# Kernel tuning notes

Hardware: AMD Instinct MI355X
Metric: run time of the kernel (lower is better)

The kernel has to match this reference:

```python
import jax, jax.numpy as jnp
import numpy as np

# Qwen3-VL-MoE text experts (training path): token permute -> grouped GEMM
# (gate_up) -> SwiGLU -> grouped GEMM (down) -> token unpermute + prob combine.
# Routing is generated perfectly balanced (each expert receives exactly M/E
# expanded tokens) so the grouped GEMM over the sorted token buffer is exactly
# a batched matmul over E contiguous groups -- same math as npu_grouped_matmul.

E, H, D, T, K = 32, 2048, 768, 4096, 8  # experts, hidden, moe_intermediate, tokens, top_k
M = T * K                                # expanded rows


def setup_inputs() -> dict:
    key = jax.random.key(0)
    k1, k2, k3, k4, k5 = jax.random.split(key, 5)
    hidden_states = jax.random.normal(k1, (T, H), dtype=jnp.float32)
    routing_weights = jax.nn.softmax(jax.random.normal(k2, (T, E), dtype=jnp.float32), axis=-1)
    # balanced expert assignment: each expert id appears exactly M // E times
    flat = jnp.tile(jnp.arange(E, dtype=jnp.int32), M // E)
    router_indices = jax.random.permutation(k3, flat).reshape(T, K)
    gate_up_proj = jax.random.normal(k4, (E, H, 2 * D), dtype=jnp.float32) * 0.02
    down_proj = jax.random.normal(k5, (E, D, H), dtype=jnp.float32) * 0.02
    return {
        "hidden_states": hidden_states,
        "routing_weights": routing_weights,
        "router_indices": router_indices,
        "gate_up_proj": gate_up_proj,
        "down_proj": down_proj,
    }


def reference(hidden_states, routing_weights, router_indices, gate_up_proj, down_proj):
    n_tok, hid = hidden_states.shape
    n_exp = gate_up_proj.shape[0]
    top_k = router_indices.shape[1]
    n_rows = n_tok * top_k
    grp = n_rows // n_exp  # balanced group size

    # --- npu_moe_token_permute: sort expanded (token, slot) rows by expert id
    flat_experts = router_indices.reshape(-1)            # (M,)
    order = jnp.argsort(flat_experts)                    # stable sort by expert
    permuted = hidden_states[order // top_k]             # (M, H)

    # --- grouped GEMM #1 (gate_up): balanced groups -> batched matmul
    xg = permuted.reshape(n_exp, grp, hid)               # (E, g, H)
    gate_up = jnp.einsum('egh,ehd->egd', xg, gate_up_proj)  # (E, g, 2D)

    # --- npu_swiglu(dim=-1): silu(first half) * second half
    gate, up = jnp.split(gate_up, 2, axis=-1)
    act = jax.nn.silu(gate) * up                         # (E, g, D)

    # --- grouped GEMM #2 (down)
    out = jnp.einsum('egd,edh->egh', act, down_proj).reshape(n_rows, hid)

    # --- npu_moe_token_unpermute: invert permutation, combine with probs
    inv = jnp.argsort(order)
    expanded = out[inv].reshape(n_tok, top_k, hid)       # (T, K, H)
    probs = jnp.take_along_axis(routing_weights, router_indices, axis=1)  # (T, K)
    return jnp.einsum('tkh,tk->th', expanded, probs)     # (T, H)
```

## Files before the change

### kernel.cpp

```cpp
#include <hip/hip_runtime.h>
#include <hip/hip_bf16.h>
#include <cstdint>


#define E_   32
#define H_   2048
#define D_   768
#define T_   4096
#define K_   8
#define M_   (T_ * K_)
#define G_   (M_ / E_)
#define GU2  (2 * D_)

typedef unsigned short u16;
typedef short bf16x8 __attribute__((ext_vector_type(8)));
typedef float f32x4 __attribute__((ext_vector_type(4)));
typedef unsigned short u16x2 __attribute__((ext_vector_type(2)));
typedef unsigned short u16x8 __attribute__((ext_vector_type(8)));

__device__ __forceinline__ u16 f2bf(float f) {
  unsigned u = __float_as_uint(f);
  u += 0x7FFFu + ((u >> 16) & 1u);
  return (u16)(u >> 16);
}
__device__ __forceinline__ float bf2f(u16 v) {
  return __uint_as_float(((unsigned)v) << 16);
}

#define GLOAD16(g, l) __builtin_amdgcn_global_load_lds(                        \
    (const __attribute__((address_space(1))) void*)(g),                        \
    (__attribute__((address_space(3))) void*)(l), 16, 0, 0)

#define VM8()   asm volatile("s_waitcnt vmcnt(8)" ::: "memory")
#define VM4()   asm volatile("s_waitcnt vmcnt(4)" ::: "memory")
#define VM0()   asm volatile("s_waitcnt vmcnt(0)" ::: "memory")
#define LGKM0() asm volatile("s_waitcnt lgkmcnt(0)" ::: "memory")
#define SCHB()  __builtin_amdgcn_sched_barrier(0)
#define BAR()   __builtin_amdgcn_s_barrier()

__global__ __launch_bounds__(256) void cvt_hidden(const float* __restrict__ in,
                                                  u16* __restrict__ out) {
  const int i = blockIdx.x * 256 + threadIdx.x;
  const float4 v = ((const float4*)in)[i];
  u16x2 a; a.x = f2bf(v.x); a.y = f2bf(v.y);
  u16x2 b; b.x = f2bf(v.z); b.y = f2bf(v.w);
  *(u16x2*)&out[(size_t)i * 4]     = a;
  *(u16x2*)&out[(size_t)i * 4 + 2] = b;
}

__global__ __launch_bounds__(256) void transpose_cvt(const float* __restrict__ in,
                                                     u16* __restrict__ out,
                                                     int R, int C, int mode) {
  __shared__ u16 tl[64 * 72];
  const int b = blockIdx.z;
  const int c0 = blockIdx.x * 64, r0 = blockIdx.y * 64;
  const int tid = threadIdx.x;
  const float* ip = in + ((size_t)b * R + r0) * C + c0;
  const int rr4 = tid >> 4;
  const int cc4 = (tid & 15) * 4;
#pragma unroll
  for (int p = 0; p < 4; ++p) {
    const int r = p * 16 + rr4;
    const float4 v = *(const float4*)&ip[(size_t)r * C + cc4];
    tl[(cc4 + 0) * 72 + r] = f2bf(v.x);
    tl[(cc4 + 1) * 72 + r] = f2bf(v.y);
    tl[(cc4 + 2) * 72 + r] = f2bf(v.z);
    tl[(cc4 + 3) * 72 + r] = f2bf(v.w);
  }
  __syncthreads();
  const int rs = (tid & 7) * 8;
#pragma unroll
  for (int q = 0; q < 2; ++q) {
    const int c = q * 32 + (tid >> 3);
    const int gc = c0 + c;
    int rr;
    if (mode == 1) {
      const int j = (gc < D_) ? gc : (gc - D_);
      rr = (j >> 4) * 32 + ((gc < D_) ? 0 : 16) + (j & 15);
    } else {
      rr = gc;
    }
    const u16x8 v = *(const u16x8*)&tl[c * 72 + rs];
    *(u16x8*)&out[((size_t)b * C + rr) * R + r0 + rs] = v;
  }
}

__global__ __launch_bounds__(256) void build_perm_fast(const int* __restrict__ ridx,
                                                       int* __restrict__ perm,
                                                       int* __restrict__ gcnt) {
  __shared__ int lc[E_];
  __shared__ int lb[E_];
  const int tid = threadIdx.x;
  if (tid < E_) lc[tid] = 0;
  __syncthreads();
  const int i = blockIdx.x * 256 + tid;
  const int e = ridx[i];
  const int p = atomicAdd(&lc[e], 1);
  __syncthreads();
  if (tid < E_) lb[tid] = atomicAdd(&gcnt[tid], lc[tid]);
  __syncthreads();
  perm[e * G_ + lb[e] + p] = i;
}

__global__ __launch_bounds__(512, 2) void gemm1_swiglu(
    const u16* __restrict__ hid, const u16* __restrict__ gup,
    const int* __restrict__ perm, u16* __restrict__ act) {
  __shared__ u16 As[4][8192];
  __shared__ u16 Bs[4][8192];
  const int NT = H_ / 32;

  const int nwg = 6 * 4 * E_;
  const int wid = (blockIdx.x % 8) * (nwg / 8) + blockIdx.x / 8;
  const int e = wid / 24;
  const int mb = (wid / 6) % 4;
  const int nb = wid % 6;

  const int tid = threadIdx.x;
  const int lane = tid & 63, w = tid >> 6;
  const int wr = w >> 2, wc = w & 3;

  const int srow = tid >> 2, schunk = tid & 3;
  const u16* pA[2]; const u16* pB[2];
#pragma unroll
  for (int q = 0; q < 2; ++q) {
    const int r = q * 128 + srow;
    const int cg = (schunk ^ ((r >> 1) & 3)) * 8;
    const int token = perm[e * G_ + mb * 256 + r] >> 3;
    pA[q] = hid + (size_t)token * H_ + cg;
    pB[q] = gup + ((size_t)e * GU2 + nb * 256 + r) * H_ + cg;
  }

  int aoff[8], boff[4];
  {
    const int l15 = lane & 15, hk = lane >> 4;
#pragma unroll
    for (int m = 0; m < 8; ++m) {
      const int rA = wr * 128 + m * 16 + l15;
      aoff[m] = rA * 32 + ((hk ^ ((rA >> 1) & 3)) * 8);
    }
#pragma unroll
    for (int n = 0; n < 4; ++n) {
      const int rB = wc * 64 + n * 16 + l15;
      boff[n] = rB * 32 + ((hk ^ ((rB >> 1) & 3)) * 8);
    }
  }

  f32x4 acc[8][4];
#pragma unroll
  for (int m = 0; m < 8; ++m)
#pragma unroll
    for (int n = 0; n < 4; ++n) acc[m][n] = (f32x4){0.f, 0.f, 0.f, 0.f};

  GLOAD16(pA[0], &As[0][tid * 8]);      GLOAD16(pA[1], &As[0][4096 + tid * 8]);
  GLOAD16(pB[0], &Bs[0][tid * 8]);      GLOAD16(pB[1], &Bs[0][4096 + tid * 8]);
  GLOAD16(pA[0] + 32, &As[1][tid * 8]); GLOAD16(pA[1] + 32, &As[1][4096 + tid * 8]);
  GLOAD16(pB[0] + 32, &Bs[1][tid * 8]); GLOAD16(pB[1] + 32, &Bs[1][4096 + tid * 8]);
  GLOAD16(pA[0] + 64, &As[2][tid * 8]); GLOAD16(pA[1] + 64, &As[2][4096 + tid * 8]);
  GLOAD16(pB[0] + 64, &Bs[2][tid * 8]); GLOAD16(pB[1] + 64, &Bs[2][4096 + tid * 8]);
  VM8(); BAR(); SCHB();

#pragma unroll 4
  for (int t = 0; t < NT; ++t) {
    const int slot = t & 3, ts = (t + 3) & 3;
    const bool st = (t + 3) < NT;
    const u16* Ab = As[slot]; const u16* Bb = Bs[slot];
    bf16x8 av[4], bv[4];
#pragma unroll
    for (int n = 0; n < 4; ++n) bv[n] = *(const bf16x8*)&Bb[boff[n]];
#pragma unroll
    for (int m = 0; m < 4; ++m) av[m] = *(const bf16x8*)&Ab[aoff[m]];
    if (st) {
      GLOAD16(pA[0] + (t + 3) * 32, &As[ts][tid * 8]);
      GLOAD16(pA[1] + (t + 3) * 32, &As[ts][4096 + tid * 8]);
    }
    SCHB(); LGKM0(); SCHB();
    __builtin_amdgcn_s_setprio(1);
#pragma unroll
    for (int m = 0; m < 4; ++m)
#pragma unroll
      for (int n = 0; n < 4; ++n)
        acc[m][n] = __builtin_amdgcn_mfma_f32_16x16x32_bf16(av[m], bv[n],
                                                            acc[m][n], 0, 0, 0);
    __builtin_amdgcn_s_setprio(0);
    SCHB();
#pragma unroll
    for (int m = 0; m < 4; ++m) av[m] = *(const bf16x8*)&Ab[aoff[m + 4]];
    if (st) {
      GLOAD16(pB[0] + (t + 3) * 32, &Bs[ts][tid * 8]);
      GLOAD16(pB[1] + (t + 3) * 32, &Bs[ts][4096 + tid * 8]);
    }
    SCHB(); LGKM0(); SCHB();
    __builtin_amdgcn_s_setprio(1);
#pragma unroll
    for (int m = 0; m < 4; ++m)
#pragma unroll
      for (int n = 0; n < 4; ++n)
        acc[m + 4][n] = __builtin_amdgcn_mfma_f32_16x16x32_bf16(av[m], bv[n],
                                                                acc[m + 4][n], 0, 0, 0);
    __builtin_amdgcn_s_setprio(0);
    SCHB();
    if (t + 3 < NT)      { VM8(); }
    else if (t + 2 < NT) { VM4(); }
    else                 { VM0(); }
    BAR(); SCHB();
  }

  const int lrow = (lane >> 4) * 4, lcol = lane & 15;
#pragma unroll
  for (int m = 0; m < 8; ++m)
#pragma unroll
    for (int p = 0; p < 2; ++p)
#pragma unroll
      for (int r = 0; r < 4; ++r) {
        const float g = acc[m][2 * p][r];
        const float u = acc[m][2 * p + 1][r];
        const float a_ = g / (1.f + __expf(-g)) * u;
        const int row = mb * 256 + wr * 128 + m * 16 + lrow + r;
        const int dcol = (nb * 8 + wc * 2 + p) * 16 + lcol;
        act[((size_t)e * G_ + row) * D_ + dcol] = f2bf(a_);
      }
}

__global__ __launch_bounds__(512, 2) void gemm2_scatter(
    const u16* __restrict__ act, const u16* __restrict__ dwn,
    const int* __restrict__ perm, u16* __restrict__ expo) {
  __shared__ u16 As[4][8192];
  __shared__ u16 Bs[4][8192];
  const int NT = D_ / 32;

  const int nwg = 8 * 4 * E_;
  const int wid = (blockIdx.x % 8) * (nwg / 8) + blockIdx.x / 8;
  const int e = wid / 32;
  const int mb = (wid / 8) % 4;
  const int nb = wid % 8;

  const int tid = threadIdx.x;
  const int lane = tid & 63, w = tid >> 6;
  const int wr = w >> 2, wc = w & 3;

  const int srow = tid >> 2, schunk = tid & 3;
  const u16* pA[2]; const u16* pB[2];
#pragma unroll
  for (int q = 0; q < 2; ++q) {
    const int r = q * 128 + srow;
    const int cg = (schunk ^ ((r >> 1) & 3)) * 8;
    pA[q] = act + ((size_t)e * G_ + mb * 256 + r) * D_ + cg;
    pB[q] = dwn + ((size_t)e * H_ + nb * 256 + r) * D_ + cg;
  }

  int aoff[8], boff[4];
  {
    const int l15 = lane & 15, hk = lane >> 4;
#pragma unroll
    for (int m = 0; m < 8; ++m) {
      const int rA = wr * 128 + m * 16 + l15;
      aoff[m] = rA * 32 + ((hk ^ ((rA >> 1) & 3)) * 8);
    }
#pragma unroll
    for (int n = 0; n < 4; ++n) {
      const int rB = wc * 64 + n * 16 + l15;
      boff[n] = rB * 32 + ((hk ^ ((rB >> 1) & 3)) * 8);
    }
  }

  f32x4 acc[8][4];
#pragma unroll
  for (int m = 0; m < 8; ++m)
#pragma unroll
    for (int n = 0; n < 4; ++n) acc[m][n] = (f32x4){0.f, 0.f, 0.f, 0.f};

  GLOAD16(pA[0], &As[0][tid * 8]);      GLOAD16(pA[1], &As[0][4096 + tid * 8]);
  GLOAD16(pB[0], &Bs[0][tid * 8]);      GLOAD16(pB[1], &Bs[0][4096 + tid * 8]);
  GLOAD16(pA[0] + 32, &As[1][tid * 8]); GLOAD16(pA[1] + 32, &As[1][4096 + tid * 8]);
  GLOAD16(pB[0] + 32, &Bs[1][tid * 8]); GLOAD16(pB[1] + 32, &Bs[1][4096 + tid * 8]);
  GLOAD16(pA[0] + 64, &As[2][tid * 8]); GLOAD16(pA[1] + 64, &As[2][4096 + tid * 8]);
  GLOAD16(pB[0] + 64, &Bs[2][tid * 8]); GLOAD16(pB[1] + 64, &Bs[2][4096 + tid * 8]);
  VM8(); BAR(); SCHB();

#pragma unroll 4
  for (int t = 0; t < NT; ++t) {
    const int slot = t & 3, ts = (t + 3) & 3;
    const bool st = (t + 3) < NT;
    const u16* Ab = As[slot]; const u16* Bb = Bs[slot];
    bf16x8 av[4], bv[4];
#pragma unroll
    for (int n = 0; n < 4; ++n) bv[n] = *(const bf16x8*)&Bb[boff[n]];
#pragma unroll
    for (int m = 0; m < 4; ++m) av[m] = *(const bf16x8*)&Ab[aoff[m]];
    if (st) {
      GLOAD16(pA[0] + (t + 3) * 32, &As[ts][tid * 8]);
      GLOAD16(pA[1] + (t + 3) * 32, &As[ts][4096 + tid * 8]);
    }
    SCHB(); LGKM0(); SCHB();
    __builtin_amdgcn_s_setprio(1);
#pragma unroll
    for (int m = 0; m < 4; ++m)
#pragma unroll
      for (int n = 0; n < 4; ++n)
        acc[m][n] = __builtin_amdgcn_mfma_f32_16x16x32_bf16(av[m], bv[n],
                                                            acc[m][n], 0, 0, 0);
    __builtin_amdgcn_s_setprio(0);
    SCHB();
#pragma unroll
    for (int m = 0; m < 4; ++m) av[m] = *(const bf16x8*)&Ab[aoff[m + 4]];
    if (st) {
      GLOAD16(pB[0] + (t + 3) * 32, &Bs[ts][tid * 8]);
      GLOAD16(pB[1] + (t + 3) * 32, &Bs[ts][4096 + tid * 8]);
    }
    SCHB(); LGKM0(); SCHB();
    __builtin_amdgcn_s_setprio(1);
#pragma unroll
    for (int m = 0; m < 4; ++m)
#pragma unroll
      for (int n = 0; n < 4; ++n)
        acc[m + 4][n] = __builtin_amdgcn_mfma_f32_16x16x32_bf16(av[m], bv[n],
                                                                acc[m + 4][n], 0, 0, 0);
    __builtin_amdgcn_s_setprio(0);
    SCHB();
    if (t + 3 < NT)      { VM8(); }
    else if (t + 2 < NT) { VM4(); }
    else                 { VM0(); }
    BAR(); SCHB();
  }

  const int lrow = (lane >> 4) * 4, lcol = lane & 15;
#pragma unroll
  for (int m = 0; m < 8; ++m)
#pragma unroll
    for (int r = 0; r < 4; ++r) {
      const int dst = e * G_ + mb * 256 + wr * 128 + m * 16 + lrow + r;
      const int src = perm[dst];
      u16* orow = expo + (size_t)src * H_ + nb * 256 + wc * 64;
#pragma unroll
      for (int n = 0; n < 4; ++n)
        orow[n * 16 + lcol] = f2bf(acc[m][n][r]);
    }
}

__global__ __launch_bounds__(256) void combine(const u16* __restrict__ expo,
                                               const int* __restrict__ ridx,
                                               const float* __restrict__ rw,
                                               float* __restrict__ out) {
  __shared__ float pr[K_];
  const int t = blockIdx.x;
  if (threadIdx.x < K_)
    pr[threadIdx.x] = rw[t * E_ + ridx[t * K_ + threadIdx.x]];
  __syncthreads();
  const int h0 = threadIdx.x * 8;
  float r[8] = {0.f, 0.f, 0.f, 0.f, 0.f, 0.f, 0.f, 0.f};
#pragma unroll
  for (int k = 0; k < K_; ++k) {
    const float p = pr[k];
    const u16x8 v = *(const u16x8*)&expo[((size_t)(t * K_ + k)) * H_ + h0];
#pragma unroll
    for (int j = 0; j < 8; ++j) r[j] += p * bf2f(v[j]);
  }
  float4 o0 = {r[0], r[1], r[2], r[3]};
  float4 o1 = {r[4], r[5], r[6], r[7]};
  *(float4*)&out[(size_t)t * H_ + h0]     = o0;
  *(float4*)&out[(size_t)t * H_ + h0 + 4] = o1;
}

extern "C" void kernel_launch(void* const* d_in, const int* in_sizes, int n_in,
                              void* d_out, int out_size, void* d_ws, size_t ws_size,
                              hipStream_t stream) {
  const float* hidden = (const float*)d_in[0];
  const float* rw     = (const float*)d_in[1];
  const int*   ridx   = (const int*)d_in[2];
  const float* gup_f  = (const float*)d_in[3];
  const float* dwn_f  = (const float*)d_in[4];
  float* out = (float*)d_out;

  char* ws = (char*)d_ws;
  size_t off = 0;
  auto alloc = [&](size_t bytes) -> void* {
    void* p = ws + off;
    off += (bytes + 255) & ~(size_t)255;
    return p;
  };
  u16*   hid_bf = (u16*)alloc((size_t)T_ * H_ * 2);
  u16*   gup_t  = (u16*)alloc((size_t)E_ * GU2 * H_ * 2);
  u16*   dwn_t  = (u16*)alloc((size_t)E_ * H_ * D_ * 2);
  u16*   act    = (u16*)alloc((size_t)M_ * D_ * 2);
  u16*   expo   = (u16*)alloc((size_t)M_ * H_ * 2);
  int*   perm   = (int*)alloc((size_t)M_ * 4);
  int*   gcnt   = (int*)alloc((size_t)E_ * 4);
  if (off > ws_size) return;

  hipMemsetAsync(gcnt, 0, E_ * sizeof(int), stream);
  cvt_hidden<<<(T_ * H_ / 4) / 256, 256, 0, stream>>>(hidden, hid_bf);
  transpose_cvt<<<dim3(GU2 / 64, H_ / 64, E_), 256, 0, stream>>>(gup_f, gup_t, H_, GU2, 1);
  transpose_cvt<<<dim3(H_ / 64, D_ / 64, E_), 256, 0, stream>>>(dwn_f, dwn_t, D_, H_, 0);
  build_perm_fast<<<M_ / 256, 256, 0, stream>>>(ridx, perm, gcnt);
  gemm1_swiglu<<<6 * 4 * E_, 512, 0, stream>>>(hid_bf, gup_t, perm, act);
  gemm2_scatter<<<8 * 4 * E_, 512, 0, stream>>>(act, dwn_t, perm, expo);
  combine<<<T_, 256, 0, stream>>>(expo, ridx, rw, out);
}
```

Before: 528.7 us.

## Software-pipeline LDS fragment reads with register double-buffering in both GEMMs

Restructures the main loop of both grouped GEMM kernels so the A/B fragments for the next K-tile are read from LDS into a second register set while the current tile's MFMAs run, ping-ponging between two register buffers. All four global-to-LDS prefetches for tile t+3 are now issued together at the start of each iteration, and the vmcnt waits are adjusted to match. The aim is to hide LDS read latency behind matrix math. The cost is more live VGPRs for the doubled fragment registers, which may lower occupancy or cause spills. The loop also assumes an even tile count.

```diff
diff --git a/kernel.cpp b/kernel.cpp
--- a/kernel.cpp
+++ b/kernel.cpp
@@ -31,12 +31,46 @@
     (const __attribute__((address_space(1))) void*)(g),                        \
     (__attribute__((address_space(3))) void*)(l), 16, 0, 0)
 
-#define VM8()   asm volatile("s_waitcnt vmcnt(8)" ::: "memory")
 #define VM4()   asm volatile("s_waitcnt vmcnt(4)" ::: "memory")
 #define VM0()   asm volatile("s_waitcnt vmcnt(0)" ::: "memory")
 #define LGKM0() asm volatile("s_waitcnt lgkmcnt(0)" ::: "memory")
 #define SCHB()  __builtin_amdgcn_sched_barrier(0)
 #define BAR()   __builtin_amdgcn_s_barrier()
+
+#define TILE_BODY(tc, AVC, BVC, AVN, BVN)                                      \
+  {                                                                            \
+    LGKM0(); SCHB();                                                           \
+    if ((tc) + 3 < NT) {                                                       \
+      const int s_ = ((tc) + 3) & 3;                                           \
+      GLOAD16(pA[0] + ((tc) + 3) * 32, &As[s_][tid * 8]);                      \
+      GLOAD16(pA[1] + ((tc) + 3) * 32, &As[s_][4096 + tid * 8]);               \
+      GLOAD16(pB[0] + ((tc) + 3) * 32, &Bs[s_][tid * 8]);                      \
+      GLOAD16(pB[1] + ((tc) + 3) * 32, &Bs[s_][4096 + tid * 8]);               \
+    }                                                                          \
+    __builtin_amdgcn_s_setprio(1);                                             \
+    _Pragma("unroll") for (int m_ = 0; m_ < 4; ++m_)                           \
+      _Pragma("unroll") for (int n_ = 0; n_ < 4; ++n_)                         \
+        acc[m_][n_] = __builtin_amdgcn_mfma_f32_16x16x32_bf16(                 \
+            AVC[m_], BVC[n_], acc[m_][n_], 0, 0, 0);                           \
+    __builtin_amdgcn_s_setprio(0);                                             \
+    if ((tc) + 1 < NT) {                                                       \
+      const u16* Abn_ = As[((tc) + 1) & 3];                                    \
+      const u16* Bbn_ = Bs[((tc) + 1) & 3];                                    \
+      _Pragma("unroll") for (int n_ = 0; n_ < 4; ++n_)                         \
+        BVN[n_] = *(const bf16x8*)&Bbn_[boff[n_]];                             \
+      _Pragma("unroll") for (int m_ = 0; m_ < 8; ++m_)                         \
+        AVN[m_] = *(const bf16x8*)&Abn_[aoff[m_]];                             \
+    }                                                                          \
+    __builtin_amdgcn_s_setprio(1);                                             \
+    _Pragma("unroll") for (int m_ = 0; m_ < 4; ++m_)                           \
+      _Pragma("unroll") for (int n_ = 0; n_ < 4; ++n_)                         \
+        acc[m_ + 4][n_] = __builtin_amdgcn_mfma_f32_16x16x32_bf16(             \
+            AVC[m_ + 4], BVC[n_], acc[m_ + 4][n_], 0, 0, 0);                   \
+    __builtin_amdgcn_s_setprio(0);                                             \
+    SCHB();                                                                    \
+    if ((tc) + 3 < NT) { VM4(); } else { VM0(); }                              \
+    BAR(); SCHB();                                                             \
+  }
 
 __global__ __launch_bounds__(256) void cvt_hidden(const float* __restrict__ in,
                                                   u16* __restrict__ out) {
@@ -157,52 +191,21 @@
   GLOAD16(pB[0] + 32, &Bs[1][tid * 8]); GLOAD16(pB[1] + 32, &Bs[1][4096 + tid * 8]);
   GLOAD16(pA[0] + 64, &As[2][tid * 8]); GLOAD16(pA[1] + 64, &As[2][4096 + tid * 8]);
   GLOAD16(pB[0] + 64, &Bs[2][tid * 8]); GLOAD16(pB[1] + 64, &Bs[2][4096 + tid * 8]);
-  VM8(); BAR(); SCHB();
-
-#pragma unroll 4
-  for (int t = 0; t < NT; ++t) {
-    const int slot = t & 3, ts = (t + 3) & 3;
-    const bool st = (t + 3) < NT;
-    const u16* Ab = As[slot]; const u16* Bb = Bs[slot];
-    bf16x8 av[4], bv[4];
-#pragma unroll
-    for (int n = 0; n < 4; ++n) bv[n] = *(const bf16x8*)&Bb[boff[n]];
-#pragma unroll
-    for (int m = 0; m < 4; ++m) av[m] = *(const bf16x8*)&Ab[aoff[m]];
-    if (st) {
-      GLOAD16(pA[0] + (t + 3) * 32, &As[ts][tid * 8]);
-      GLOAD16(pA[1] + (t + 3) * 32, &As[ts][4096 + tid * 8]);
-    }
-    SCHB(); LGKM0(); SCHB();
-    __builtin_amdgcn_s_setprio(1);
-#pragma unroll
-    for (int m = 0; m < 4; ++m)
-#pragma unroll
-      for (int n = 0; n < 4; ++n)
-        acc[m][n] = __builtin_amdgcn_mfma_f32_16x16x32_bf16(av[m], bv[n],
-                                                            acc[m][n], 0, 0, 0);
-    __builtin_amdgcn_s_setprio(0);
-    SCHB();
-#pragma unroll
-    for (int m = 0; m < 4; ++m) av[m] = *(const bf16x8*)&Ab[aoff[m + 4]];
-    if (st) {
-      GLOAD16(pB[0] + (t + 3) * 32, &Bs[ts][tid * 8]);
-      GLOAD16(pB[1] + (t + 3) * 32, &Bs[ts][4096 + tid * 8]);
-    }
-    SCHB(); LGKM0(); SCHB();
-    __builtin_amdgcn_s_setprio(1);
-#pragma unroll
-    for (int m = 0; m < 4; ++m)
-#pragma unroll
-      for (int n = 0; n < 4; ++n)
-        acc[m + 4][n] = __builtin_amdgcn_mfma_f32_16x16x32_bf16(av[m], bv[n],
-                                                                acc[m + 4][n], 0, 0, 0);
-    __builtin_amdgcn_s_setprio(0);
-    SCHB();
-    if (t + 3 < NT)      { VM8(); }
-    else if (t + 2 < NT) { VM4(); }
-    else                 { VM0(); }
-    BAR(); SCHB();
+  VM4(); BAR(); SCHB();
+
+  bf16x8 av0[8], bv0[4], av1[8], bv1[4];
+  {
+    const u16* Ab = As[0]; const u16* Bb = Bs[0];
+#pragma unroll
+    for (int n = 0; n < 4; ++n) bv0[n] = *(const bf16x8*)&Bb[boff[n]];
+#pragma unroll
+    for (int m = 0; m < 8; ++m) av0[m] = *(const bf16x8*)&Ab[aoff[m]];
+  }
+
+#pragma unroll 2
+  for (int t = 0; t < NT; t += 2) {
+    TILE_BODY(t,     av0, bv0, av1, bv1);
+    TILE_BODY(t + 1, av1, bv1, av0, bv0);
   }
 
   const int lrow = (lane >> 4) * 4, lcol = lane & 15;
@@ -275,52 +278,21 @@
   GLOAD16(pB[0] + 32, &Bs[1][tid * 8]); GLOAD16(pB[1] + 32, &Bs[1][4096 + tid * 8]);
   GLOAD16(pA[0] + 64, &As[2][tid * 8]); GLOAD16(pA[1] + 64, &As[2][4096 + tid * 8]);
   GLOAD16(pB[0] + 64, &Bs[2][tid * 8]); GLOAD16(pB[1] + 64, &Bs[2][4096 + tid * 8]);
-  VM8(); BAR(); SCHB();
-
-#pragma unroll 4
-  for (int t = 0; t < NT; ++t) {
-    const int slot = t & 3, ts = (t + 3) & 3;
-    const bool st = (t + 3) < NT;
-    const u16* Ab = As[slot]; const u16* Bb = Bs[slot];
-    bf16x8 av[4], bv[4];
-#pragma unroll
-    for (int n = 0; n < 4; ++n) bv[n] = *(const bf16x8*)&Bb[boff[n]];
-#pragma unroll
-    for (int m = 0; m < 4; ++m) av[m] = *(const bf16x8*)&Ab[aoff[m]];
-    if (st) {
-      GLOAD16(pA[0] + (t + 3) * 32, &As[ts][tid * 8]);
-      GLOAD16(pA[1] + (t + 3) * 32, &As[ts][4096 + tid * 8]);
-    }
-    SCHB(); LGKM0(); SCHB();
-    __builtin_amdgcn_s_setprio(1);
-#pragma unroll
-    for (int m = 0; m < 4; ++m)
-#pragma unroll
-      for (int n = 0; n < 4; ++n)
-        acc[m][n] = __builtin_amdgcn_mfma_f32_16x16x32_bf16(av[m], bv[n],
-                                                            acc[m][n], 0, 0, 0);
-    __builtin_amdgcn_s_setprio(0);
-    SCHB();
-#pragma unroll
-    for (int m = 0; m < 4; ++m) av[m] = *(const bf16x8*)&Ab[aoff[m + 4]];
-    if (st) {
-      GLOAD16(pB[0] + (t + 3) * 32, &Bs[ts][tid * 8]);
-      GLOAD16(pB[1] + (t + 3) * 32, &Bs[ts][4096 + tid * 8]);
-    }
-    SCHB(); LGKM0(); SCHB();
-    __builtin_amdgcn_s_setprio(1);
-#pragma unroll
-    for (int m = 0; m < 4; ++m)
-#pragma unroll
-      for (int n = 0; n < 4; ++n)
-        acc[m + 4][n] = __builtin_amdgcn_mfma_f32_16x16x32_bf16(av[m], bv[n],
-                                                                acc[m + 4][n], 0, 0, 0);
-    __builtin_amdgcn_s_setprio(0);
-    SCHB();
-    if (t + 3 < NT)      { VM8(); }
-    else if (t + 2 < NT) { VM4(); }
-    else                 { VM0(); }
-    BAR(); SCHB();
+  VM4(); BAR(); SCHB();
+
+  bf16x8 av0[8], bv0[4], av1[8], bv1[4];
+  {
+    const u16* Ab = As[0]; const u16* Bb = Bs[0];
+#pragma unroll
+    for (int n = 0; n < 4; ++n) bv0[n] = *(const bf16x8*)&Bb[boff[n]];
+#pragma unroll
+    for (int m = 0; m < 8; ++m) av0[m] = *(const bf16x8*)&Ab[aoff[m]];
+  }
+
+#pragma unroll 2
+  for (int t = 0; t < NT; t += 2) {
+    TILE_BODY(t,     av0, bv0, av1, bv1);
+    TILE_BODY(t + 1, av1, bv1, av0, bv0);
   }
 
   const int lrow = (lane >> 4) * 4, lcol = lane & 15;
```

Result: slower. 1.794 ms (+239.3%).

## Fuse prep kernels and overlap down_proj transpose with gate_up GEMM

Applied to the files above, without the earlier changes.

The hidden-state cast, the gate_up transpose/convert and the permutation build are merged into one launch that picks its role from the block index. The down_proj transpose/convert moves into gemm1 as four extra producer warps, so its memory traffic runs alongside the MFMA loop. To stay in lockstep, the producer warps issue the same number of block barriers as the compute warps. This saves several launches and hides the transpose's bandwidth cost, but raises the block size to 768 threads and adds LDS, which may constrain registers or contend for memory bandwidth with the GEMM.

```diff
diff --git a/kernel.cpp b/kernel.cpp
--- a/kernel.cpp
+++ b/kernel.cpp
@@ -38,187 +38,221 @@
 #define SCHB()  __builtin_amdgcn_sched_barrier(0)
 #define BAR()   __builtin_amdgcn_s_barrier()
 
-__global__ __launch_bounds__(256) void cvt_hidden(const float* __restrict__ in,
-                                                  u16* __restrict__ out) {
-  const int i = blockIdx.x * 256 + threadIdx.x;
-  const float4 v = ((const float4*)in)[i];
-  u16x2 a; a.x = f2bf(v.x); a.y = f2bf(v.y);
-  u16x2 b; b.x = f2bf(v.z); b.y = f2bf(v.w);
-  *(u16x2*)&out[(size_t)i * 4]     = a;
-  *(u16x2*)&out[(size_t)i * 4 + 2] = b;
-}
-
-__global__ __launch_bounds__(256) void transpose_cvt(const float* __restrict__ in,
-                                                     u16* __restrict__ out,
-                                                     int R, int C, int mode) {
+__global__ __launch_bounds__(256) void prep_fused(
+    const float* __restrict__ hidden, u16* __restrict__ hid_bf,
+    const float* __restrict__ gup_f, u16* __restrict__ gup_t,
+    const int* __restrict__ ridx, int* __restrict__ perm,
+    int* __restrict__ gcnt) {
   __shared__ u16 tl[64 * 72];
-  const int b = blockIdx.z;
-  const int c0 = blockIdx.x * 64, r0 = blockIdx.y * 64;
-  const int tid = threadIdx.x;
-  const float* ip = in + ((size_t)b * R + r0) * C + c0;
-  const int rr4 = tid >> 4;
-  const int cc4 = (tid & 15) * 4;
-#pragma unroll
-  for (int p = 0; p < 4; ++p) {
-    const int r = p * 16 + rr4;
-    const float4 v = *(const float4*)&ip[(size_t)r * C + cc4];
-    tl[(cc4 + 0) * 72 + r] = f2bf(v.x);
-    tl[(cc4 + 1) * 72 + r] = f2bf(v.y);
-    tl[(cc4 + 2) * 72 + r] = f2bf(v.z);
-    tl[(cc4 + 3) * 72 + r] = f2bf(v.w);
-  }
-  __syncthreads();
-  const int rs = (tid & 7) * 8;
-#pragma unroll
-  for (int q = 0; q < 2; ++q) {
-    const int c = q * 32 + (tid >> 3);
-    const int gc = c0 + c;
-    int rr;
-    if (mode == 1) {
-      const int j = (gc < D_) ? gc : (gc - D_);
-      rr = (j >> 4) * 32 + ((gc < D_) ? 0 : 16) + (j & 15);
-    } else {
-      rr = gc;
-    }
-    const u16x8 v = *(const u16x8*)&tl[c * 72 + rs];
-    *(u16x8*)&out[((size_t)b * C + rr) * R + r0 + rs] = v;
-  }
-}
-
-__global__ __launch_bounds__(256) void build_perm_fast(const int* __restrict__ ridx,
-                                                       int* __restrict__ perm,
-                                                       int* __restrict__ gcnt) {
   __shared__ int lc[E_];
   __shared__ int lb[E_];
+  const int bid = blockIdx.x;
   const int tid = threadIdx.x;
-  if (tid < E_) lc[tid] = 0;
-  __syncthreads();
-  const int i = blockIdx.x * 256 + tid;
-  const int e = ridx[i];
-  const int p = atomicAdd(&lc[e], 1);
-  __syncthreads();
-  if (tid < E_) lb[tid] = atomicAdd(&gcnt[tid], lc[tid]);
-  __syncthreads();
-  perm[e * G_ + lb[e] + p] = i;
-}
-
-__global__ __launch_bounds__(512, 2) void gemm1_swiglu(
+  if (bid < 24576) {
+    const int bx = bid % 24, by = (bid / 24) % 32, bz = bid / 768;
+    const int c0 = bx * 64, r0 = by * 64;
+    const float* ip = gup_f + ((size_t)bz * H_ + r0) * GU2 + c0;
+    const int rr4 = tid >> 4;
+    const int cc4 = (tid & 15) * 4;
+#pragma unroll
+    for (int p = 0; p < 4; ++p) {
+      const int r = p * 16 + rr4;
+      const float4 v = *(const float4*)&ip[(size_t)r * GU2 + cc4];
+      tl[(cc4 + 0) * 72 + r] = f2bf(v.x);
+      tl[(cc4 + 1) * 72 + r] = f2bf(v.y);
+      tl[(cc4 + 2) * 72 + r] = f2bf(v.z);
+      tl[(cc4 + 3) * 72 + r] = f2bf(v.w);
+    }
+    __syncthreads();
+    const int rs = (tid & 7) * 8;
+#pragma unroll
+    for (int q = 0; q < 2; ++q) {
+      const int c = q * 32 + (tid >> 3);
+      const int gc = c0 + c;
+      const int j = (gc < D_) ? gc : (gc - D_);
+      const int rr = (j >> 4) * 32 + ((gc < D_) ? 0 : 16) + (j & 15);
+      const u16x8 v = *(const u16x8*)&tl[c * 72 + rs];
+      *(u16x8*)&gup_t[((size_t)bz * GU2 + rr) * H_ + r0 + rs] = v;
+    }
+  } else if (bid < 24576 + 8192) {
+    const int i = (bid - 24576) * 256 + tid;
+    const float4 v = ((const float4*)hidden)[i];
+    u16x2 a; a.x = f2bf(v.x); a.y = f2bf(v.y);
+    u16x2 b; b.x = f2bf(v.z); b.y = f2bf(v.w);
+    *(u16x2*)&hid_bf[(size_t)i * 4]     = a;
+    *(u16x2*)&hid_bf[(size_t)i * 4 + 2] = b;
+  } else {
+    const int blk = bid - 32768;
+    if (tid < E_) lc[tid] = 0;
+    __syncthreads();
+    const int i = blk * 256 + tid;
+    const int e = ridx[i];
+    const int p = atomicAdd(&lc[e], 1);
+    __syncthreads();
+    if (tid < E_) lb[tid] = atomicAdd(&gcnt[tid], lc[tid]);
+    __syncthreads();
+    perm[e * G_ + lb[e] + p] = i;
+  }
+}
+
+__global__ __launch_bounds__(768, 1) void gemm1_swiglu(
     const u16* __restrict__ hid, const u16* __restrict__ gup,
-    const int* __restrict__ perm, u16* __restrict__ act) {
+    const int* __restrict__ perm, u16* __restrict__ act,
+    const float* __restrict__ dwn_f, u16* __restrict__ dwn_t) {
   __shared__ u16 As[4][8192];
   __shared__ u16 Bs[4][8192];
+  __shared__ u16 Ts[64 * 72];
   const int NT = H_ / 32;
 
-  const int nwg = 6 * 4 * E_;
-  const int wid = (blockIdx.x % 8) * (nwg / 8) + blockIdx.x / 8;
-  const int e = wid / 24;
-  const int mb = (wid / 6) % 4;
-  const int nb = wid % 6;
-
   const int tid = threadIdx.x;
-  const int lane = tid & 63, w = tid >> 6;
-  const int wr = w >> 2, wc = w & 3;
-
-  const int srow = tid >> 2, schunk = tid & 3;
-  const u16* pA[2]; const u16* pB[2];
-#pragma unroll
-  for (int q = 0; q < 2; ++q) {
-    const int r = q * 128 + srow;
-    const int cg = (schunk ^ ((r >> 1) & 3)) * 8;
-    const int token = perm[e * G_ + mb * 256 + r] >> 3;
-    pA[q] = hid + (size_t)token * H_ + cg;
-    pB[q] = gup + ((size_t)e * GU2 + nb * 256 + r) * H_ + cg;
-  }
-
-  int aoff[8], boff[4];
-  {
-    const int l15 = lane & 15, hk = lane >> 4;
-#pragma unroll
-    for (int m = 0; m < 8; ++m) {
-      const int rA = wr * 128 + m * 16 + l15;
-      aoff[m] = rA * 32 + ((hk ^ ((rA >> 1) & 3)) * 8);
-    }
-#pragma unroll
-    for (int n = 0; n < 4; ++n) {
-      const int rB = wc * 64 + n * 16 + l15;
-      boff[n] = rB * 32 + ((hk ^ ((rB >> 1) & 3)) * 8);
-    }
-  }
-
-  f32x4 acc[8][4];
-#pragma unroll
-  for (int m = 0; m < 8; ++m)
-#pragma unroll
-    for (int n = 0; n < 4; ++n) acc[m][n] = (f32x4){0.f, 0.f, 0.f, 0.f};
-
-  GLOAD16(pA[0], &As[0][tid * 8]);      GLOAD16(pA[1], &As[0][4096 + tid * 8]);
-  GLOAD16(pB[0], &Bs[0][tid * 8]);      GLOAD16(pB[1], &Bs[0][4096 + tid * 8]);
-  GLOAD16(pA[0] + 32, &As[1][tid * 8]); GLOAD16(pA[1] + 32, &As[1][4096 + tid * 8]);
-  GLOAD16(pB[0] + 32, &Bs[1][tid * 8]); GLOAD16(pB[1] + 32, &Bs[1][4096 + tid * 8]);
-  GLOAD16(pA[0] + 64, &As[2][tid * 8]); GLOAD16(pA[1] + 64, &As[2][4096 + tid * 8]);
-  GLOAD16(pB[0] + 64, &Bs[2][tid * 8]); GLOAD16(pB[1] + 64, &Bs[2][4096 + tid * 8]);
-  VM8(); BAR(); SCHB();
+  const int w = tid >> 6;
+
+  if (w < 8) {
+    const int nwg = 6 * 4 * E_;
+    const int wid = (blockIdx.x % 8) * (nwg / 8) + blockIdx.x / 8;
+    const int e = wid / 24;
+    const int mb = (wid / 6) % 4;
+    const int nb = wid % 6;
+
+    const int lane = tid & 63;
+    const int wr = w >> 2, wc = w & 3;
+
+    const int srow = tid >> 2, schunk = tid & 3;
+    const u16* pA[2]; const u16* pB[2];
+#pragma unroll
+    for (int q = 0; q < 2; ++q) {
+      const int r = q * 128 + srow;
+      const int cg = (schunk ^ ((r >> 1) & 3)) * 8;
+      const int token = perm[e * G_ + mb * 256 + r] >> 3;
+      pA[q] = hid + (size_t)token * H_ + cg;
+      pB[q] = gup + ((size_t)e * GU2 + nb * 256 + r) * H_ + cg;
+    }
+
+    int aoff[8], boff[4];
+    {
+      const int l15 = lane & 15, hk = lane >> 4;
+#pragma unroll
+      for (int m = 0; m < 8; ++m) {
+        const int rA = wr * 128 + m * 16 + l15;
+        aoff[m] = rA * 32 + ((hk ^ ((rA >> 1) & 3)) * 8);
+      }
+#pragma unroll
+      for (int n = 0; n < 4; ++n) {
+        const int rB = wc * 64 + n * 16 + l15;
+        boff[n] = rB * 32 + ((hk ^ ((rB >> 1) & 3)) * 8);
+      }
+    }
+
+    f32x4 acc[8][4];
+#pragma unroll
+    for (int m = 0; m < 8; ++m)
+#pragma unroll
+      for (int n = 0; n < 4; ++n) acc[m][n] = (f32x4){0.f, 0.f, 0.f, 0.f};
+
+    GLOAD16(pA[0], &As[0][tid * 8]);      GLOAD16(pA[1], &As[0][4096 + tid * 8]);
+    GLOAD16(pB[0], &Bs[0][tid * 8]);      GLOAD16(pB[1], &Bs[0][4096 + tid * 8]);
+    GLOAD16(pA[0] + 32, &As[1][tid * 8]); GLOAD16(pA[1] + 32, &As[1][4096 + tid * 8]);
+    GLOAD16(pB[0] + 32, &Bs[1][tid * 8]); GLOAD16(pB[1] + 32, &Bs[1][4096 + tid * 8]);
+    GLOAD16(pA[0] + 64, &As[2][tid * 8]); GLOAD16(pA[1] + 64, &As[2][4096 + tid * 8]);
+    GLOAD16(pB[0] + 64, &Bs[2][tid * 8]); GLOAD16(pB[1] + 64, &Bs[2][4096 + tid * 8]);
+    VM8(); BAR(); SCHB();
 
 #pragma unroll 4
-  for (int t = 0; t < NT; ++t) {
-    const int slot = t & 3, ts = (t + 3) & 3;
-    const bool st = (t + 3) < NT;
-    const u16* Ab = As[slot]; const u16* Bb = Bs[slot];
-    bf16x8 av[4], bv[4];
-#pragma unroll
-    for (int n = 0; n < 4; ++n) bv[n] = *(const bf16x8*)&Bb[boff[n]];
-#pragma unroll
-    for (int m = 0; m < 4; ++m) av[m] = *(const bf16x8*)&Ab[aoff[m]];
-    if (st) {
-      GLOAD16(pA[0] + (t + 3) * 32, &As[ts][tid * 8]);
-      GLOAD16(pA[1] + (t + 3) * 32, &As[ts][4096 + tid * 8]);
-    }
-    SCHB(); LGKM0(); SCHB();
-    __builtin_amdgcn_s_setprio(1);
-#pragma unroll
-    for (int m = 0; m < 4; ++m)
-#pragma unroll
-      for (int n = 0; n < 4; ++n)
-        acc[m][n] = __builtin_amdgcn_mfma_f32_16x16x32_bf16(av[m], bv[n],
-                                                            acc[m][n], 0, 0, 0);
-    __builtin_amdgcn_s_setprio(0);
-    SCHB();
-#pragma unroll
-    for (int m = 0; m < 4; ++m) av[m] = *(const bf16x8*)&Ab[aoff[m + 4]];
-    if (st) {
-      GLOAD16(pB[0] + (t + 3) * 32, &Bs[ts][tid * 8]);
-      GLOAD16(pB[1] + (t + 3) * 32, &Bs[ts][4096 + tid * 8]);
-    }
-    SCHB(); LGKM0(); SCHB();
-    __builtin_amdgcn_s_setprio(1);
-#pragma unroll
-    for (int m = 0; m < 4; ++m)
-#pragma unroll
-      for (int n = 0; n < 4; ++n)
-        acc[m + 4][n] = __builtin_amdgcn_mfma_f32_16x16x32_bf16(av[m], bv[n],
-                                                                acc[m + 4][n], 0, 0, 0);
-    __builtin_amdgcn_s_setprio(0);
-    SCHB();
-    if (t + 3 < NT)      { VM8(); }
-    else if (t + 2 < NT) { VM4(); }
-    else                 { VM0(); }
-    BAR(); SCHB();
-  }
-
-  const int lrow = (lane >> 4) * 4, lcol = lane & 15;
-#pragma unroll
-  for (int m = 0; m < 8; ++m)
-#pragma unroll
-    for (int p = 0; p < 2; ++p)
-#pragma unroll
-      for (int r = 0; r < 4; ++r) {
-        const float g = acc[m][2 * p][r];
-        const float u = acc[m][2 * p + 1][r];
-        const float a_ = g / (1.f + __expf(-g)) * u;
-        const int row = mb * 256 + wr * 128 + m * 16 + lrow + r;
-        const int dcol = (nb * 8 + wc * 2 + p) * 16 + lcol;
-        act[((size_t)e * G_ + row) * D_ + dcol] = f2bf(a_);
+    for (int t = 0; t < NT; ++t) {
+      const int slot = t & 3, ts = (t + 3) & 3;
+      const bool st = (t + 3) < NT;
+      const u16* Ab = As[slot]; const u16* Bb = Bs[slot];
+      bf16x8 av[4], bv[4];
+#pragma unroll
+      for (int n = 0; n < 4; ++n) bv[n] = *(const bf16x8*)&Bb[boff[n]];
+#pragma unroll
+      for (int m = 0; m < 4; ++m) av[m] = *(const bf16x8*)&Ab[aoff[m]];
+      if (st) {
+        GLOAD16(pA[0] + (t + 3) * 32, &As[ts][tid * 8]);
+        GLOAD16(pA[1] + (t + 3) * 32, &As[ts][4096 + tid * 8]);
       }
+      SCHB(); LGKM0(); SCHB();
+      __builtin_amdgcn_s_setprio(1);
+#pragma unroll
+      for (int m = 0; m < 4; ++m)
+#pragma unroll
+        for (int n = 0; n < 4; ++n)
+          acc[m][n] = __builtin_amdgcn_mfma_f32_16x16x32_bf16(av[m], bv[n],
+                                                              acc[m][n], 0, 0, 0);
+      __builtin_amdgcn_s_setprio(0);
+      SCHB();
+#pragma unroll
+      for (int m = 0; m < 4; ++m) av[m] = *(const bf16x8*)&Ab[aoff[m + 4]];
+      if (st) {
+        GLOAD16(pB[0] + (t + 3) * 32, &Bs[ts][tid * 8]);
+        GLOAD16(pB[1] + (t + 3) * 32, &Bs[ts][4096 + tid * 8]);
+      }
+      SCHB(); LGKM0(); SCHB();
+      __builtin_amdgcn_s_setprio(1);
+#pragma unroll
+      for (int m = 0; m < 4; ++m)
+#pragma unroll
+        for (int n = 0; n < 4; ++n)
+          acc[m + 4][n] = __builtin_amdgcn_mfma_f32_16x16x32_bf16(av[m], bv[n],
+                                                                  acc[m + 4][n], 0, 0, 0);
+      __builtin_amdgcn_s_setprio(0);
+      SCHB();
+      if (t + 3 < NT)      { VM8(); }
+      else if (t + 2 < NT) { VM4(); }
+      else                 { VM0(); }
+      BAR(); SCHB();
+    }
+
+    const int lrow = (lane >> 4) * 4, lcol = lane & 15;
+#pragma unroll
+    for (int m = 0; m < 8; ++m)
+#pragma unroll
+      for (int p = 0; p < 2; ++p)
+#pragma unroll
+        for (int r = 0; r < 4; ++r) {
+          const float g = acc[m][2 * p][r];
+          const float u = acc[m][2 * p + 1][r];
+          const float a_ = g / (1.f + __expf(-g)) * u;
+          const int row = mb * 256 + wr * 128 + m * 16 + lrow + r;
+          const int dcol = (nb * 8 + wc * 2 + p) * 16 + lcol;
+          act[((size_t)e * G_ + row) * D_ + dcol] = f2bf(a_);
+        }
+  } else {
+    const int tid2 = tid - 512;
+    const int rr4 = tid2 >> 4;
+    const int cc4 = (tid2 & 15) * 4;
+    const int rs  = (tid2 & 7) * 8;
+    const int cdr = tid2 >> 3;
+    for (int i = 0; i < NT + 1; ++i) {
+      if (i < 32) {
+        const int j = blockIdx.x * 16 + (i >> 1);
+        const int cx = j & 31;
+        const int ry = (j >> 5) % 12;
+        const int ez = j / 384;
+        if ((i & 1) == 0) {
+          const float* ip = dwn_f + ((size_t)(ez * D_ + ry * 64)) * H_ + cx * 64;
+#pragma unroll
+          for (int p = 0; p < 4; ++p) {
+            const int r = p * 16 + rr4;
+            const float4 v = *(const float4*)&ip[(size_t)r * H_ + cc4];
+            Ts[(cc4 + 0) * 72 + r] = f2bf(v.x);
+            Ts[(cc4 + 1) * 72 + r] = f2bf(v.y);
+            Ts[(cc4 + 2) * 72 + r] = f2bf(v.z);
+            Ts[(cc4 + 3) * 72 + r] = f2bf(v.w);
+          }
+        } else {
+#pragma unroll
+          for (int q = 0; q < 2; ++q) {
+            const int c = q * 32 + cdr;
+            const u16x8 v = *(const u16x8*)&Ts[c * 72 + rs];
+            *(u16x8*)&dwn_t[((size_t)ez * H_ + cx * 64 + c) * D_ + ry * 64 + rs] = v;
+          }
+        }
+      }
+      LGKM0(); SCHB();
+      BAR();
+    }
+  }
 }
 
 __global__ __launch_bounds__(512, 2) void gemm2_scatter(
@@ -388,11 +422,10 @@
   if (off > ws_size) return;
 
   hipMemsetAsync(gcnt, 0, E_ * sizeof(int), stream);
-  cvt_hidden<<<(T_ * H_ / 4) / 256, 256, 0, stream>>>(hidden, hid_bf);
-  transpose_cvt<<<dim3(GU2 / 64, H_ / 64, E_), 256, 0, stream>>>(gup_f, gup_t, H_, GU2, 1);
-  transpose_cvt<<<dim3(H_ / 64, D_ / 64, E_), 256, 0, stream>>>(dwn_f, dwn_t, D_, H_, 0);
-  build_perm_fast<<<M_ / 256, 256, 0, stream>>>(ridx, perm, gcnt);
-  gemm1_swiglu<<<6 * 4 * E_, 512, 0, stream>>>(hid_bf, gup_t, perm, act);
+  prep_fused<<<24576 + 8192 + 128, 256, 0, stream>>>(hidden, hid_bf, gup_f,
+                                                     gup_t, ridx, perm, gcnt);
+  gemm1_swiglu<<<6 * 4 * E_, 768, 0, stream>>>(hid_bf, gup_t, perm, act,
+                                               dwn_f, dwn_t);
   gemm2_scatter<<<8 * 4 * E_, 512, 0, stream>>>(act, dwn_t, perm, expo);
   combine<<<T_, 256, 0, stream>>>(expo, ridx, rw, out);
 }
```

New measurement: 1.495 ms. 183% more time.
